# Kernel optimization log

Hardware: AMD Instinct MI355X
Metric: run time of the kernel (lower is better)

## Reference

```python
import jax, jax.numpy as jnp
import numpy as np
from jax import lax

B, N = 16, 8192          # batch, points per cloud
G, K = 512, 32           # num_groups, group_size
TOKEN_DIM = 384
BN_EPS = 1e-5


def setup_inputs() -> dict:
    key = jax.random.key(0)
    ks = jax.random.split(key, 8)
    w = lambda i, shape: jax.random.normal(ks[i], shape, jnp.float32) * 0.05
    return {
        "points": jax.random.normal(ks[0], (B, N, 3), jnp.float32),
        # first_conv: Conv1d(3,128,1,bias=False) -> BN(128) -> ReLU -> Conv1d(128,256,1)
        "w1": w(1, (128, 3)),
        "bn1_gamma": jnp.ones((128,), jnp.float32),
        "bn1_beta": jnp.zeros((128,), jnp.float32),
        "bn1_mean": jnp.zeros((128,), jnp.float32),
        "bn1_var": jnp.ones((128,), jnp.float32),
        "w2": w(2, (256, 128)),
        "b2": jnp.zeros((256,), jnp.float32),
        # second_conv: Conv1d(512,512,1,bias=False) -> BN(512) -> ReLU -> Conv1d(512,384,1)
        "w3": w(3, (512, 512)),
        "bn2_gamma": jnp.ones((512,), jnp.float32),
        "bn2_beta": jnp.zeros((512,), jnp.float32),
        "bn2_mean": jnp.zeros((512,), jnp.float32),
        "bn2_var": jnp.ones((512,), jnp.float32),
        "w4": w(4, (TOKEN_DIM, 512)),
        "b4": jnp.zeros((TOKEN_DIM,), jnp.float32),
    }


def _fps(xyz, num_samples):
    """Farthest point sampling. xyz: [B,N,3] -> idx [B,num_samples] (start = point 0)."""
    b, n, _ = xyz.shape
    start = jnp.zeros((b,), jnp.int32)
    init_min = jnp.full((b, n), 1e10, xyz.dtype)

    def body(carry, _):
        min_d2, last = carry
        last_pt = jnp.take_along_axis(xyz, last[:, None, None], axis=1)  # [B,1,3]
        d2 = jnp.sum((xyz - last_pt) ** 2, axis=-1)                      # [B,N]
        min_d2 = jnp.minimum(min_d2, d2)
        nxt = jnp.argmax(min_d2, axis=-1).astype(jnp.int32)
        return (min_d2, nxt), last

    _, idx = lax.scan(body, (init_min, start), None, length=num_samples)
    return idx.T  # [B,num_samples]


def _bn(x, gamma, beta, mean, var):
    # inference batchnorm over last (channel) axis
    return (x - mean) * lax.rsqrt(var + BN_EPS) * gamma + beta


def reference(points, w1, bn1_gamma, bn1_beta, bn1_mean, bn1_var, w2, b2,
              w3, bn2_gamma, bn2_beta, bn2_mean, bn2_var, w4, b4):
    xyz = points[:, :, :3]
    fidx = _fps(xyz, G)                                       # [B,G]
    centers = jnp.take_along_axis(xyz, fidx[:, :, None], 1)   # [B,G,3]

    # brute-force KNN via squared distances [B,G,N]
    pn = jnp.sum(xyz * xyz, -1)                               # [B,N]
    cn = jnp.sum(centers * centers, -1)                       # [B,G]
    d2 = cn[:, :, None] + pn[:, None, :] - 2.0 * jnp.einsum('bgc,bnc->bgn', centers, xyz)
    _, idx = lax.top_k(-d2, K)                                # [B,G,K] nearest indices

    groups = jax.vmap(lambda p, i: p[i])(points, idx)          # [B,G,K,3]
    groups = groups - centers[:, :, None, :]                   # center-relative coords

    x = groups.reshape(B * G, K, 3)                            # [M,K,3]
    # first_conv
    f = jnp.einsum('mkc,dc->mkd', x, w1)                       # [M,K,128]
    f = jax.nn.relu(_bn(f, bn1_gamma, bn1_beta, bn1_mean, bn1_var))
    f = jnp.einsum('mkd,ed->mke', f, w2) + b2                  # [M,K,256]
    g = jnp.max(f, axis=1, keepdims=True)                      # [M,1,256]
    f = jnp.concatenate([jnp.broadcast_to(g, f.shape), f], -1) # [M,K,512]
    # second_conv
    f = jnp.einsum('mke,fe->mkf', f, w3)                       # [M,K,512]
    f = jax.nn.relu(_bn(f, bn2_gamma, bn2_beta, bn2_mean, bn2_var))
    f = jnp.einsum('mkf,of->mko', f, w4) + b4                  # [M,K,384]
    tokens = jnp.max(f, axis=1).reshape(B, G, TOKEN_DIM)
    return tokens, centers
```

## Files before the change

### kernel.cpp

```cpp
#include <hip/hip_runtime.h>
#include <stdint.h>

#define PB 16
#define PN 8192
#define PG 512
#define PK 32
#define PTOK 384
#define PM (PB*PG)
#define PMK (PM*PK)
static constexpr float BN_EPS_C = 1e-5f;

typedef short bh8  __attribute__((ext_vector_type(8)));
typedef float f32x4 __attribute__((ext_vector_type(4)));

__device__ __forceinline__ short f2bf(float f){
  unsigned u = __float_as_uint(f);
  unsigned r = u + 0x7fffu + ((u>>16)&1u);
  return (short)(r>>16);
}
__device__ __forceinline__ float bf2f(short s){
  return __uint_as_float(((unsigned)(unsigned short)s)<<16);
}
__device__ __forceinline__ void gload16(const void* g, void* l){
  __builtin_amdgcn_global_load_lds((const __attribute__((address_space(1))) unsigned int*)g,
                                   (__attribute__((address_space(3))) unsigned int*)l,
                                   16, 0, 0);
}

__global__ __launch_bounds__(1024, 4) void fps_kernel(const float* __restrict__ points,
                                                      float* __restrict__ centers){
#pragma clang fp contract(off)
  const int b = blockIdx.x;
  const int t = threadIdx.x;
  const float* P = points + (size_t)b*PN*3;
  __shared__ float4 Lc[PN];
  __shared__ unsigned short sidx[PN];
  __shared__ int shist[512];
  __shared__ int spart[64];
  __shared__ unsigned long long swa[3];
  if (t < 512) shist[t] = 0;
  if (t < 3)   swa[t] = 0ull;
  __syncthreads();
  int mycell[8];
#pragma unroll
  for (int i=0;i<8;i++){
    int j = i*1024 + t;
    float x=P[j*3+0], y=P[j*3+1], z=P[j*3+2];
    Lc[j] = make_float4(x,y,z,0.f);
    int qx=(int)fminf(fmaxf((x+4.f)*1.0f,0.f),7.f);
    int qy=(int)fminf(fmaxf((y+4.f)*1.0f,0.f),7.f);
    int qz=(int)fminf(fmaxf((z+4.f)*1.0f,0.f),7.f);
    int mc = (qx&1)|((qx&2)<<2)|((qx&4)<<4)
           | ((qy&1)<<1)|((qy&2)<<3)|((qy&4)<<5)
           | ((qz&1)<<2)|((qz&2)<<4)|((qz&4)<<6);
    mycell[i]=mc;
    atomicAdd(&shist[mc],1);
  }
  __syncthreads();
  if (t < 64){
    int acc=0;
#pragma unroll
    for (int k=0;k<8;k++){ int h=shist[t*8+k]; shist[t*8+k]=acc; acc+=h; }
    spart[t]=acc;
  }
  __syncthreads();
  if (t==0){ int acc=0; for (int k=0;k<64;k++){ int h=spart[k]; spart[k]=acc; acc+=h; } }
  __syncthreads();
  if (t < 64){
    int off=spart[t];
#pragma unroll
    for (int k=0;k<8;k++) shist[t*8+k] += off;
  }
  __syncthreads();
#pragma unroll
  for (int i=0;i<8;i++){
    int j = i*1024 + t;
    int r = atomicAdd(&shist[mycell[i]],1);
    sidx[r] = (unsigned short)j;
  }
  __syncthreads();
  float px[8],py[8],pz[8],md[8]; int lowc[8];
  float tlx=1e30f,tly=1e30f,tlz=1e30f,thx=-1e30f,thy=-1e30f,thz=-1e30f;
#pragma unroll
  for (int i=0;i<8;i++){
    int oj = sidx[t*8+i];
    float4 p4 = Lc[oj];
    float x=p4.x, y=p4.y, z=p4.z;
    px[i]=x; py[i]=y; pz[i]=z; md[i]=1e10f; lowc[i]=PN-1-oj;
    tlx=fminf(tlx,x); thx=fmaxf(thx,x);
    tly=fminf(tly,y); thy=fmaxf(thy,y);
    tlz=fminf(tlz,z); thz=fmaxf(thz,z);
  }
#pragma unroll
  for (int off=32; off; off>>=1){
    tlx=fminf(tlx,__shfl_xor(tlx,off)); thx=fmaxf(thx,__shfl_xor(thx,off));
    tly=fminf(tly,__shfl_xor(tly,off)); thy=fmaxf(thy,__shfl_xor(thy,off));
    tlz=fminf(tlz,__shfl_xor(tlz,off)); thz=fmaxf(thz,__shfl_xor(thz,off));
  }
  unsigned long long wkey = ((unsigned long long)0x7F800000u)<<32;
  float cx=P[0], cy=P[1], cz=P[2];
  if (t==0){ float* c = centers + (size_t)b*PG*3; c[0]=cx; c[1]=cy; c[2]=cz; }
  const int lane = t & 63;
  __syncthreads();
  for (int g=1; g<PG; g++){
    const int sl = g%3, ns = (g+1)%3;
    float ddx=fmaxf(fmaxf(tlx-cx, cx-thx),0.f);
    float ddy=fmaxf(fmaxf(tly-cy, cy-thy),0.f);
    float ddz=fmaxf(fmaxf(tlz-cz, cz-thz),0.f);
    float dmin2=((ddx*ddx+ddy*ddy)+ddz*ddz)*0.999999f;
    if (!(dmin2 >= __uint_as_float((unsigned)(wkey>>32)))){
      unsigned long long bk = 0ull;
#pragma unroll
      for (int i=0;i<8;i++){
        float dx=px[i]-cx, dy=py[i]-cy, dz=pz[i]-cz;
        float d2 = (dx*dx + dy*dy) + dz*dz;
        md[i] = fminf(md[i], d2);
        unsigned long long ki = ((unsigned long long)__float_as_uint(md[i])<<32)
                              | (unsigned)lowc[i];
        if (ki > bk) bk = ki;
      }
#pragma unroll
      for (int mask=32; mask; mask>>=1){
        unsigned long long o = __shfl_xor(bk, mask);
        if (o > bk) bk = o;
      }
      wkey = bk;
    }
    if (lane==0) atomicMax(&swa[sl], wkey);
    if (t==0) swa[ns] = 0ull;
    __syncthreads();
    unsigned long long w = swa[sl];
    int j = PN-1 - (int)(w & 0xFFFFFFFFu);
    float4 c4 = Lc[j];
    cx = c4.x; cy = c4.y; cz = c4.z;
    if (t==0){ float* cc = centers + ((size_t)b*PG + g)*3; cc[0]=cx; cc[1]=cy; cc[2]=cz; }
  }
}

__global__ __launch_bounds__(256) void knn_kernel(const float* __restrict__ points,
                                                  const float* __restrict__ centers,
                                                  float* __restrict__ groups){
#pragma clang fp contract(off)
  const int m = blockIdx.x;
  const int b = m >> 9;
  const int t = threadIdx.x;
  const float* P = points + (size_t)b*PN*3;
  const float* c = centers + (size_t)m*3;
  const float cx=c[0], cy=c[1], cz=c[2];
  const float cn = (cx*cx + cy*cy) + cz*cz;
  unsigned long long key[PK];
#pragma unroll
  for (int i=0;i<PK;i++){
    int j = i*256 + t;
    float x=P[j*3+0], y=P[j*3+1], z=P[j*3+2];
    float pn = (x*x + y*y) + z*z;
    float e  = (cx*x + cy*y) + cz*z;
    float d2 = (cn + pn) - 2.0f*e;
    unsigned u = __float_as_uint(d2);
    u ^= (u & 0x80000000u) ? 0xFFFFFFFFu : 0x80000000u;
    key[i] = ((unsigned long long)u << 32) | (unsigned)j;
  }
  unsigned long long lmin = key[0];
#pragma unroll
  for (int i=1;i<PK;i++) if (key[i] < lmin) lmin = key[i];
  __shared__ unsigned long long swk[2][4];
  __shared__ int s_idx[PK];
  const int lane = t & 63, wid = t >> 6;
  for (int it=0; it<PK; it++){
    unsigned long long v = lmin;
#pragma unroll
    for (int off=32; off; off>>=1){
      unsigned long long o = __shfl_down(v, off);
      if (o < v) v = o;
    }
    if (lane==0) swk[it&1][wid] = v;
    __syncthreads();
    unsigned long long w = swk[it&1][0];
#pragma unroll
    for (int q=1;q<4;q++) if (swk[it&1][q] < w) w = swk[it&1][q];
    int wj = (int)(w & 0xFFFFFFFFull);
    if (t==0) s_idx[it] = wj;
    if ((wj & 255) == t){
#pragma unroll
      for (int i=0;i<PK;i++) if (key[i] == w) key[i] = ~0ull;
      lmin = key[0];
#pragma unroll
      for (int i=1;i<PK;i++) if (key[i] < lmin) lmin = key[i];
    }
  }
  __syncthreads();
  if (t < PK*3){
    int k = t/3, cc = t - k*3;
    int j = s_idx[k];
    groups[((size_t)m*PK + k)*3 + cc] = P[j*3+cc] - c[cc];
  }
}

__global__ __launch_bounds__(512, 2) void mlp_kernel(const float* __restrict__ grp,
                                                     const float* __restrict__ w1,
                                                     const float* __restrict__ sc1,
                                                     const float* __restrict__ sh1,
                                                     const short* __restrict__ w2b,
                                                     const float* __restrict__ b2,
                                                     const short* __restrict__ w3ab,
                                                     const short* __restrict__ w3bb,
                                                     const float* __restrict__ sc2,
                                                     const float* __restrict__ sh2,
                                                     const short* __restrict__ w4b,
                                                     const float* __restrict__ b4,
                                                     float* __restrict__ tokens){
  __shared__ __align__(16) short s_f1f3[16384];
  __shared__ __align__(16) short s_f2[32768];
  __shared__ __align__(16) short s_g[1024];
  __shared__ __align__(16) short s_bst[24576];
  const int t = threadIdx.x;
  const int lane = t & 63, wid = t >> 6;
  const int mh = wid >> 1, nq = wid & 1;
  const int B0 = blockIdx.x * 128;
  const int G0 = blockIdx.x * 4;
  const int srow = lane >> 2;
  const int scol = (lane & 3) * 8;
  const int frow = lane & 15;
  const int fk   = (lane >> 4) * 8;
  const int rb   = (lane >> 4) * 4;
  const int cb   = lane & 15;

  {
    int r = t & 127, dg = t >> 7;
    float x0 = grp[(size_t)(B0+r)*3 + 0];
    float x1 = grp[(size_t)(B0+r)*3 + 1];
    float x2 = grp[(size_t)(B0+r)*3 + 2];
#pragma unroll
    for (int dd=0; dd<32; dd++){
      int d = dg*32 + dd;
      float a = x0*w1[d*3+0] + x1*w1[d*3+1] + x2*w1[d*3+2];
      float y = a*sc1[d] + sh1[d];
      s_f1f3[dg*4096 + r*32 + dd] = f2bf(fmaxf(y, 0.f));
    }
  }
  __syncthreads();

  {
    f32x4 accB[2][8] = {};
    for (int k0=0; k0<128; k0+=64){
      for (int cc=wid; cc<32; cc+=8){
        int sub = cc & 1, rc = cc >> 1;
        int r = rc*16 + srow;
        gload16(w2b + (size_t)r*128 + k0 + sub*32 + scol, &s_bst[sub*8192 + rc*512]);
      }
      __syncthreads();
#pragma unroll
      for (int sub=0; sub<2; sub++){
        int kc = (k0 + sub*32) >> 5;
        bh8 af[2], bf[8];
#pragma unroll
        for (int i=0;i<2;i++)
          af[i] = *(const bh8*)&s_f1f3[kc*4096 + (mh*32 + i*16 + frow)*32 + fk];
#pragma unroll
        for (int j=0;j<8;j++)
          bf[j] = *(const bh8*)&s_bst[sub*8192 + (nq*128 + j*16 + frow)*32 + fk];
#pragma unroll
        for (int i=0;i<2;i++)
#pragma unroll
          for (int j=0;j<8;j++)
            accB[i][j] = __builtin_amdgcn_mfma_f32_16x16x32_bf16(af[i], bf[j], accB[i][j], 0,0,0);
      }
      __syncthreads();
    }
#pragma unroll
    for (int i=0;i<2;i++)
#pragma unroll
      for (int j=0;j<8;j++){
        int col = nq*128 + j*16 + cb;
#pragma unroll
        for (int r=0;r<4;r++){
          int row = mh*32 + i*16 + rb + r;
          s_f2[(col>>5)*4096 + row*32 + (col&31)] = f2bf(accB[i][j][r] + b2[col]);
        }
      }
  }
  __syncthreads();

  {
#pragma unroll
    for (int task=0; task<2; task++){
      int g = (t>>8) + task*2;
      int col = t & 255;
      int kc = col >> 5, c5 = col & 31;
      float mx = -3.4e38f;
#pragma unroll
      for (int kk=0; kk<PK; kk++)
        mx = fmaxf(mx, bf2f(s_f2[kc*4096 + (g*32 + kk)*32 + c5]));
      s_g[g*256 + col] = f2bf(mx);
    }
  }
  __syncthreads();

  f32x4 acc4[2][12] = {};
  for (int nc=0; nc<4; nc++){
    f32x4 acc3[2][4] = {};
    for (int k0=0; k0<512; k0+=64){
      const short* w3s = (k0 < 256) ? w3ab : w3bb;
      int kk0 = (k0 < 256) ? k0 : (k0 - 256);
      for (int cc=wid; cc<16; cc+=8){
        int sub = cc & 1, rc = cc >> 1;
        int r = nc*128 + rc*16 + srow;
        gload16(w3s + (size_t)r*256 + kk0 + sub*32 + scol, &s_bst[sub*4096 + rc*512]);
      }
      __syncthreads();
#pragma unroll
      for (int sub=0; sub<2; sub++){
        int k = k0 + sub*32;
        bh8 af[2], bf[4];
        if (k < 256){
#pragma unroll
          for (int i=0;i<2;i++)
            af[i] = *(const bh8*)&s_g[mh*256 + k + fk];
        } else {
          int kc = (k - 256) >> 5;
#pragma unroll
          for (int i=0;i<2;i++)
            af[i] = *(const bh8*)&s_f2[kc*4096 + (mh*32 + i*16 + frow)*32 + fk];
        }
#pragma unroll
        for (int j=0;j<4;j++)
          bf[j] = *(const bh8*)&s_bst[sub*4096 + (nq*64 + j*16 + frow)*32 + fk];
#pragma unroll
        for (int i=0;i<2;i++)
#pragma unroll
          for (int j=0;j<4;j++)
            acc3[i][j] = __builtin_amdgcn_mfma_f32_16x16x32_bf16(af[i], bf[j], acc3[i][j], 0,0,0);
      }
      __syncthreads();
    }
#pragma unroll
    for (int i=0;i<2;i++)
#pragma unroll
      for (int j=0;j<4;j++){
        int cl = nq*64 + j*16 + cb;
        int f  = nc*128 + cl;
        float s = sc2[f], h = sh2[f];
#pragma unroll
        for (int r=0;r<4;r++){
          int row = mh*32 + i*16 + rb + r;
          float v = acc3[i][j][r]*s + h;
          s_f1f3[(cl>>5)*4096 + row*32 + (cl&31)] = f2bf(fmaxf(v, 0.f));
        }
      }
    __syncthreads();
    for (int kk0=0; kk0<128; kk0+=64){
      for (int cc=wid; cc<48; cc+=8){
        int sub = cc & 1, rc = cc >> 1;
        int r = rc*16 + srow;
        gload16(w4b + (size_t)r*512 + nc*128 + kk0 + sub*32 + scol, &s_bst[sub*12288 + rc*512]);
      }
      __syncthreads();
#pragma unroll
      for (int sub=0; sub<2; sub++){
        int kc = (kk0 + sub*32) >> 5;
        bh8 af[2], bf[12];
#pragma unroll
        for (int i=0;i<2;i++)
          af[i] = *(const bh8*)&s_f1f3[kc*4096 + (mh*32 + i*16 + frow)*32 + fk];
#pragma unroll
        for (int j=0;j<12;j++)
          bf[j] = *(const bh8*)&s_bst[sub*12288 + (nq*192 + j*16 + frow)*32 + fk];
#pragma unroll
        for (int i=0;i<2;i++)
#pragma unroll
          for (int j=0;j<12;j++)
            acc4[i][j] = __builtin_amdgcn_mfma_f32_16x16x32_bf16(af[i], bf[j], acc4[i][j], 0,0,0);
      }
      __syncthreads();
    }
  }

#pragma unroll
  for (int j=0;j<12;j++){
    int col = nq*192 + j*16 + cb;
    float mx = -3.4e38f;
#pragma unroll
    for (int i=0;i<2;i++)
#pragma unroll
      for (int r=0;r<4;r++)
        mx = fmaxf(mx, acc4[i][j][r]);
    mx = fmaxf(mx, __shfl_xor(mx, 16));
    mx = fmaxf(mx, __shfl_xor(mx, 32));
    if (lane < 16)
      tokens[(size_t)(G0 + mh)*PTOK + col] = mx + b4[col];
  }
}

__global__ __launch_bounds__(256) void prep_kernel(const float* __restrict__ w2,
    const float* __restrict__ w3, const float* __restrict__ w4,
    const float* __restrict__ g1, const float* __restrict__ be1,
    const float* __restrict__ mu1, const float* __restrict__ va1,
    const float* __restrict__ g2, const float* __restrict__ be2,
    const float* __restrict__ mu2, const float* __restrict__ va2,
    short* __restrict__ w2b, short* __restrict__ w3ab, short* __restrict__ w3bb,
    short* __restrict__ w4b, float* __restrict__ sc1, float* __restrict__ sh1,
    float* __restrict__ sc2, float* __restrict__ sh2){
  int i = blockIdx.x*256 + threadIdx.x;
  if (i < 256*128) w2b[i] = f2bf(w2[i]);
  if (i < 512*512){
    int f = i >> 9, e = i & 511;
    short v = f2bf(w3[i]);
    if (e < 256) w3ab[f*256 + e] = v; else w3bb[f*256 + (e-256)] = v;
  }
  if (i < 384*512) w4b[i] = f2bf(w4[i]);
  if (i < 128){ float s = g1[i]*rsqrtf(va1[i] + BN_EPS_C); sc1[i]=s; sh1[i]=be1[i]-mu1[i]*s; }
  if (i < 512){ float s = g2[i]*rsqrtf(va2[i] + BN_EPS_C); sc2[i]=s; sh2[i]=be2[i]-mu2[i]*s; }
}

extern "C" void kernel_launch(void* const* d_in, const int* in_sizes, int n_in,
                              void* d_out, int out_size, void* d_ws, size_t ws_size,
                              hipStream_t stream){
  const float* points = (const float*)d_in[0];
  const float* w1  = (const float*)d_in[1];
  const float* g1  = (const float*)d_in[2];
  const float* be1 = (const float*)d_in[3];
  const float* mu1 = (const float*)d_in[4];
  const float* va1 = (const float*)d_in[5];
  const float* w2  = (const float*)d_in[6];
  const float* b2  = (const float*)d_in[7];
  const float* w3  = (const float*)d_in[8];
  const float* g2  = (const float*)d_in[9];
  const float* be2 = (const float*)d_in[10];
  const float* mu2 = (const float*)d_in[11];
  const float* va2 = (const float*)d_in[12];
  const float* w4  = (const float*)d_in[13];
  const float* b4  = (const float*)d_in[14];
  float* tokens  = (float*)d_out;
  float* centers = (float*)d_out + (size_t)PM*PTOK;

  char* ws = (char*)d_ws;
  float* grp  = (float*)(ws + 0);
  short* w2b  = (short*)(ws + 3145728ull);
  short* w3ab = (short*)(ws + 3211264ull);
  short* w3bb = (short*)(ws + 3473408ull);
  short* w4b  = (short*)(ws + 3735552ull);
  float* sc1  = (float*)(ws + 4128768ull);
  float* sh1  = (float*)(ws + 4129280ull);
  float* sc2  = (float*)(ws + 4129792ull);
  float* sh2  = (float*)(ws + 4131840ull);

  prep_kernel<<<1024, 256, 0, stream>>>(w2, w3, w4, g1, be1, mu1, va1, g2, be2, mu2, va2,
                                        w2b, w3ab, w3bb, w4b, sc1, sh1, sc2, sh2);
  fps_kernel<<<PB, 1024, 0, stream>>>(points, centers);
  knn_kernel<<<PM, 256, 0, stream>>>(points, centers, grp);
  mlp_kernel<<<PMK/128, 512, 0, stream>>>(grp, w1, sc1, sh1, w2b, b2,
                                          w3ab, w3bb, sc2, sh2, w4b, b4, tokens);
}
```

Before: 1.220 ms.

## Fuse FPS, KNN and MLP into persistent megakernel with progress-flag streaming

Replaces the three separate FPS, KNN and MLP launches with one persistent kernel. Sixteen blocks run FPS and publish per-batch progress counters every four centers. The remaining worker blocks pull tasks from an atomic queue, spin until their centers are ready, then do KNN for four groups and the MLP in the same block, with the tile reshaped for 16 waves. This overlaps the long serial FPS with downstream work and removes the intermediate groups buffer. In exchange it relies on forward progress of co-resident blocks and spin-waiting, and the larger block with fewer waves per SIMD may reduce MLP efficiency.

```diff
diff --git a/kernel.cpp b/kernel.cpp
--- a/kernel.cpp
+++ b/kernel.cpp
@@ -8,6 +8,8 @@
 #define PTOK 384
 #define PM (PB*PG)
 #define PMK (PM*PK)
+#define NWORK 224
+#define NTASK (PM/4)
 static constexpr float BN_EPS_C = 1e-5f;
 
 typedef short bh8  __attribute__((ext_vector_type(8)));
@@ -27,265 +29,282 @@
                                    16, 0, 0);
 }
 
-__global__ __launch_bounds__(1024, 4) void fps_kernel(const float* __restrict__ points,
-                                                      float* __restrict__ centers){
+__global__ __launch_bounds__(1024) void mega_kernel(
+    const float* __restrict__ points, float* __restrict__ centers,
+    int* __restrict__ prog, int* __restrict__ qhead,
+    const float* __restrict__ w1, const float* __restrict__ sc1,
+    const float* __restrict__ sh1, const short* __restrict__ w2b,
+    const float* __restrict__ b2, const short* __restrict__ w3ab,
+    const short* __restrict__ w3bb, const float* __restrict__ sc2,
+    const float* __restrict__ sh2, const short* __restrict__ w4b,
+    const float* __restrict__ b4, float* __restrict__ tokens){
 #pragma clang fp contract(off)
-  const int b = blockIdx.x;
-  const int t = threadIdx.x;
-  const float* P = points + (size_t)b*PN*3;
-  __shared__ float4 Lc[PN];
-  __shared__ unsigned short sidx[PN];
-  __shared__ int shist[512];
-  __shared__ int spart[64];
-  __shared__ unsigned long long swa[3];
-  if (t < 512) shist[t] = 0;
-  if (t < 3)   swa[t] = 0ull;
-  __syncthreads();
-  int mycell[8];
-#pragma unroll
-  for (int i=0;i<8;i++){
-    int j = i*1024 + t;
-    float x=P[j*3+0], y=P[j*3+1], z=P[j*3+2];
-    Lc[j] = make_float4(x,y,z,0.f);
-    int qx=(int)fminf(fmaxf((x+4.f)*1.0f,0.f),7.f);
-    int qy=(int)fminf(fmaxf((y+4.f)*1.0f,0.f),7.f);
-    int qz=(int)fminf(fmaxf((z+4.f)*1.0f,0.f),7.f);
-    int mc = (qx&1)|((qx&2)<<2)|((qx&4)<<4)
-           | ((qy&1)<<1)|((qy&2)<<3)|((qy&4)<<5)
-           | ((qz&1)<<2)|((qz&2)<<4)|((qz&4)<<6);
-    mycell[i]=mc;
-    atomicAdd(&shist[mc],1);
-  }
-  __syncthreads();
-  if (t < 64){
-    int acc=0;
-#pragma unroll
-    for (int k=0;k<8;k++){ int h=shist[t*8+k]; shist[t*8+k]=acc; acc+=h; }
-    spart[t]=acc;
-  }
-  __syncthreads();
-  if (t==0){ int acc=0; for (int k=0;k<64;k++){ int h=spart[k]; spart[k]=acc; acc+=h; } }
-  __syncthreads();
-  if (t < 64){
-    int off=spart[t];
-#pragma unroll
-    for (int k=0;k<8;k++) shist[t*8+k] += off;
-  }
-  __syncthreads();
-#pragma unroll
-  for (int i=0;i<8;i++){
-    int j = i*1024 + t;
-    int r = atomicAdd(&shist[mycell[i]],1);
-    sidx[r] = (unsigned short)j;
-  }
-  __syncthreads();
-  float px[8],py[8],pz[8],md[8]; int lowc[8];
-  float tlx=1e30f,tly=1e30f,tlz=1e30f,thx=-1e30f,thy=-1e30f,thz=-1e30f;
-#pragma unroll
-  for (int i=0;i<8;i++){
-    int oj = sidx[t*8+i];
-    float4 p4 = Lc[oj];
-    float x=p4.x, y=p4.y, z=p4.z;
-    px[i]=x; py[i]=y; pz[i]=z; md[i]=1e10f; lowc[i]=PN-1-oj;
-    tlx=fminf(tlx,x); thx=fmaxf(thx,x);
-    tly=fminf(tly,y); thy=fmaxf(thy,y);
-    tlz=fminf(tlz,z); thz=fmaxf(thz,z);
-  }
-#pragma unroll
-  for (int off=32; off; off>>=1){
-    tlx=fminf(tlx,__shfl_xor(tlx,off)); thx=fmaxf(thx,__shfl_xor(thx,off));
-    tly=fminf(tly,__shfl_xor(tly,off)); thy=fmaxf(thy,__shfl_xor(thy,off));
-    tlz=fminf(tlz,__shfl_xor(tlz,off)); thz=fmaxf(thz,__shfl_xor(thz,off));
-  }
-  unsigned long long wkey = ((unsigned long long)0x7F800000u)<<32;
-  float cx=P[0], cy=P[1], cz=P[2];
-  if (t==0){ float* c = centers + (size_t)b*PG*3; c[0]=cx; c[1]=cy; c[2]=cz; }
-  const int lane = t & 63;
-  __syncthreads();
-  for (int g=1; g<PG; g++){
-    const int sl = g%3, ns = (g+1)%3;
-    float ddx=fmaxf(fmaxf(tlx-cx, cx-thx),0.f);
-    float ddy=fmaxf(fmaxf(tly-cy, cy-thy),0.f);
-    float ddz=fmaxf(fmaxf(tlz-cz, cz-thz),0.f);
-    float dmin2=((ddx*ddx+ddy*ddy)+ddz*ddz)*0.999999f;
-    if (!(dmin2 >= __uint_as_float((unsigned)(wkey>>32)))){
-      unsigned long long bk = 0ull;
-#pragma unroll
-      for (int i=0;i<8;i++){
-        float dx=px[i]-cx, dy=py[i]-cy, dz=pz[i]-cz;
-        float d2 = (dx*dx + dy*dy) + dz*dz;
-        md[i] = fminf(md[i], d2);
-        unsigned long long ki = ((unsigned long long)__float_as_uint(md[i])<<32)
-                              | (unsigned)lowc[i];
-        if (ki > bk) bk = ki;
-      }
-#pragma unroll
-      for (int mask=32; mask; mask>>=1){
-        unsigned long long o = __shfl_xor(bk, mask);
-        if (o > bk) bk = o;
-      }
-      wkey = bk;
-    }
-    if (lane==0) atomicMax(&swa[sl], wkey);
-    if (t==0) swa[ns] = 0ull;
-    __syncthreads();
-    unsigned long long w = swa[sl];
-    int j = PN-1 - (int)(w & 0xFFFFFFFFu);
-    float4 c4 = Lc[j];
-    cx = c4.x; cy = c4.y; cz = c4.z;
-    if (t==0){ float* cc = centers + ((size_t)b*PG + g)*3; cc[0]=cx; cc[1]=cy; cc[2]=cz; }
-  }
-}
-
-__global__ __launch_bounds__(256) void knn_kernel(const float* __restrict__ points,
-                                                  const float* __restrict__ centers,
-                                                  float* __restrict__ groups){
-#pragma clang fp contract(off)
-  const int m = blockIdx.x;
-  const int b = m >> 9;
-  const int t = threadIdx.x;
-  const float* P = points + (size_t)b*PN*3;
-  const float* c = centers + (size_t)m*3;
-  const float cx=c[0], cy=c[1], cz=c[2];
-  const float cn = (cx*cx + cy*cy) + cz*cz;
-  unsigned long long key[PK];
-#pragma unroll
-  for (int i=0;i<PK;i++){
-    int j = i*256 + t;
-    float x=P[j*3+0], y=P[j*3+1], z=P[j*3+2];
-    float pn = (x*x + y*y) + z*z;
-    float e  = (cx*x + cy*y) + cz*z;
-    float d2 = (cn + pn) - 2.0f*e;
-    unsigned u = __float_as_uint(d2);
-    u ^= (u & 0x80000000u) ? 0xFFFFFFFFu : 0x80000000u;
-    key[i] = ((unsigned long long)u << 32) | (unsigned)j;
-  }
-  unsigned long long lmin = key[0];
-#pragma unroll
-  for (int i=1;i<PK;i++) if (key[i] < lmin) lmin = key[i];
-  __shared__ unsigned long long swk[2][4];
-  __shared__ int s_idx[PK];
-  const int lane = t & 63, wid = t >> 6;
-  for (int it=0; it<PK; it++){
-    unsigned long long v = lmin;
-#pragma unroll
-    for (int off=32; off; off>>=1){
-      unsigned long long o = __shfl_down(v, off);
-      if (o < v) v = o;
-    }
-    if (lane==0) swk[it&1][wid] = v;
-    __syncthreads();
-    unsigned long long w = swk[it&1][0];
-#pragma unroll
-    for (int q=1;q<4;q++) if (swk[it&1][q] < w) w = swk[it&1][q];
-    int wj = (int)(w & 0xFFFFFFFFull);
-    if (t==0) s_idx[it] = wj;
-    if ((wj & 255) == t){
-#pragma unroll
-      for (int i=0;i<PK;i++) if (key[i] == w) key[i] = ~0ull;
-      lmin = key[0];
-#pragma unroll
-      for (int i=1;i<PK;i++) if (key[i] < lmin) lmin = key[i];
-    }
-  }
-  __syncthreads();
-  if (t < PK*3){
-    int k = t/3, cc = t - k*3;
-    int j = s_idx[k];
-    groups[((size_t)m*PK + k)*3 + cc] = P[j*3+cc] - c[cc];
-  }
-}
-
-__global__ __launch_bounds__(512, 2) void mlp_kernel(const float* __restrict__ grp,
-                                                     const float* __restrict__ w1,
-                                                     const float* __restrict__ sc1,
-                                                     const float* __restrict__ sh1,
-                                                     const short* __restrict__ w2b,
-                                                     const float* __restrict__ b2,
-                                                     const short* __restrict__ w3ab,
-                                                     const short* __restrict__ w3bb,
-                                                     const float* __restrict__ sc2,
-                                                     const float* __restrict__ sh2,
-                                                     const short* __restrict__ w4b,
-                                                     const float* __restrict__ b4,
-                                                     float* __restrict__ tokens){
-  __shared__ __align__(16) short s_f1f3[16384];
-  __shared__ __align__(16) short s_f2[32768];
-  __shared__ __align__(16) short s_g[1024];
-  __shared__ __align__(16) short s_bst[24576];
+  __shared__ __align__(16) char SMEM[150528];
   const int t = threadIdx.x;
   const int lane = t & 63, wid = t >> 6;
-  const int mh = wid >> 1, nq = wid & 1;
-  const int B0 = blockIdx.x * 128;
-  const int G0 = blockIdx.x * 4;
-  const int srow = lane >> 2;
-  const int scol = (lane & 3) * 8;
-  const int frow = lane & 15;
-  const int fk   = (lane >> 4) * 8;
-  const int rb   = (lane >> 4) * 4;
-  const int cb   = lane & 15;
-
-  {
-    int r = t & 127, dg = t >> 7;
-    float x0 = grp[(size_t)(B0+r)*3 + 0];
-    float x1 = grp[(size_t)(B0+r)*3 + 1];
-    float x2 = grp[(size_t)(B0+r)*3 + 2];
-#pragma unroll
-    for (int dd=0; dd<32; dd++){
-      int d = dg*32 + dd;
-      float a = x0*w1[d*3+0] + x1*w1[d*3+1] + x2*w1[d*3+2];
-      float y = a*sc1[d] + sh1[d];
-      s_f1f3[dg*4096 + r*32 + dd] = f2bf(fmaxf(y, 0.f));
-    }
+
+  if (blockIdx.x < PB){
+    const int b = blockIdx.x;
+    const float* P = points + (size_t)b*PN*3;
+    float4* Lc = (float4*)SMEM;
+    unsigned short* sidx = (unsigned short*)(SMEM + 131072);
+    int* shist = (int*)(SMEM + 147456);
+    int* spart = (int*)(SMEM + 149504);
+    unsigned long long* swa = (unsigned long long*)(SMEM + 149760);
+    if (t < 512) shist[t] = 0;
+    if (t < 3)   swa[t] = 0ull;
+    __syncthreads();
+    int mycell[8];
+#pragma unroll
+    for (int i=0;i<8;i++){
+      int j = i*1024 + t;
+      float x=P[j*3+0], y=P[j*3+1], z=P[j*3+2];
+      Lc[j] = make_float4(x,y,z,0.f);
+      int qx=(int)fminf(fmaxf((x+4.f)*1.0f,0.f),7.f);
+      int qy=(int)fminf(fmaxf((y+4.f)*1.0f,0.f),7.f);
+      int qz=(int)fminf(fmaxf((z+4.f)*1.0f,0.f),7.f);
+      int mc = (qx&1)|((qx&2)<<2)|((qx&4)<<4)
+             | ((qy&1)<<1)|((qy&2)<<3)|((qy&4)<<5)
+             | ((qz&1)<<2)|((qz&2)<<4)|((qz&4)<<6);
+      mycell[i]=mc;
+      atomicAdd(&shist[mc],1);
+    }
+    __syncthreads();
+    if (t < 64){
+      int acc=0;
+#pragma unroll
+      for (int k=0;k<8;k++){ int h=shist[t*8+k]; shist[t*8+k]=acc; acc+=h; }
+      spart[t]=acc;
+    }
+    __syncthreads();
+    if (t==0){ int acc=0; for (int k=0;k<64;k++){ int h=spart[k]; spart[k]=acc; acc+=h; } }
+    __syncthreads();
+    if (t < 64){
+      int off=spart[t];
+#pragma unroll
+      for (int k=0;k<8;k++) shist[t*8+k] += off;
+    }
+    __syncthreads();
+#pragma unroll
+    for (int i=0;i<8;i++){
+      int j = i*1024 + t;
+      int r = atomicAdd(&shist[mycell[i]],1);
+      sidx[r] = (unsigned short)j;
+    }
+    __syncthreads();
+    float px[8],py[8],pz[8],md[8]; int lowc[8];
+    float tlx=1e30f,tly=1e30f,tlz=1e30f,thx=-1e30f,thy=-1e30f,thz=-1e30f;
+#pragma unroll
+    for (int i=0;i<8;i++){
+      int oj = sidx[t*8+i];
+      float4 p4 = Lc[oj];
+      float x=p4.x, y=p4.y, z=p4.z;
+      px[i]=x; py[i]=y; pz[i]=z; md[i]=1e10f; lowc[i]=PN-1-oj;
+      tlx=fminf(tlx,x); thx=fmaxf(thx,x);
+      tly=fminf(tly,y); thy=fmaxf(thy,y);
+      tlz=fminf(tlz,z); thz=fmaxf(thz,z);
+    }
+#pragma unroll
+    for (int off=32; off; off>>=1){
+      tlx=fminf(tlx,__shfl_xor(tlx,off)); thx=fmaxf(thx,__shfl_xor(thx,off));
+      tly=fminf(tly,__shfl_xor(tly,off)); thy=fmaxf(thy,__shfl_xor(thy,off));
+      tlz=fminf(tlz,__shfl_xor(tlz,off)); thz=fmaxf(thz,__shfl_xor(thz,off));
+    }
+    unsigned long long wkey = ((unsigned long long)0x7F800000u)<<32;
+    float cx=P[0], cy=P[1], cz=P[2];
+    if (t==0){ float* c = centers + (size_t)b*PG*3; c[0]=cx; c[1]=cy; c[2]=cz; }
+    __syncthreads();
+    for (int g=1; g<PG; g++){
+      const int sl = g%3, ns = (g+1)%3;
+      float ddx=fmaxf(fmaxf(tlx-cx, cx-thx),0.f);
+      float ddy=fmaxf(fmaxf(tly-cy, cy-thy),0.f);
+      float ddz=fmaxf(fmaxf(tlz-cz, cz-thz),0.f);
+      float dmin2=((ddx*ddx+ddy*ddy)+ddz*ddz)*0.999999f;
+      if (!(dmin2 >= __uint_as_float((unsigned)(wkey>>32)))){
+        unsigned long long bk = 0ull;
+#pragma unroll
+        for (int i=0;i<8;i++){
+          float dx=px[i]-cx, dy=py[i]-cy, dz=pz[i]-cz;
+          float d2 = (dx*dx + dy*dy) + dz*dz;
+          md[i] = fminf(md[i], d2);
+          unsigned long long ki = ((unsigned long long)__float_as_uint(md[i])<<32)
+                                | (unsigned)lowc[i];
+          if (ki > bk) bk = ki;
+        }
+#pragma unroll
+        for (int mask=32; mask; mask>>=1){
+          unsigned long long o = __shfl_xor(bk, mask);
+          if (o > bk) bk = o;
+        }
+        wkey = bk;
+      }
+      if (lane==0) atomicMax(&swa[sl], wkey);
+      if (t==0) swa[ns] = 0ull;
+      __syncthreads();
+      unsigned long long w = swa[sl];
+      int j = PN-1 - (int)(w & 0xFFFFFFFFu);
+      float4 c4 = Lc[j];
+      cx = c4.x; cy = c4.y; cz = c4.z;
+      if (t==0){
+        float* cc = centers + ((size_t)b*PG + g)*3;
+        cc[0]=cx; cc[1]=cy; cc[2]=cz;
+        if ((g & 3) == 3)
+          __hip_atomic_store(prog + b, g + 1, __ATOMIC_RELEASE, __HIP_MEMORY_SCOPE_AGENT);
+      }
+    }
+    return;
   }
-  __syncthreads();
-
-  {
-    f32x4 accB[2][8] = {};
-    for (int k0=0; k0<128; k0+=64){
-      for (int cc=wid; cc<32; cc+=8){
-        int sub = cc & 1, rc = cc >> 1;
-        int r = rc*16 + srow;
-        gload16(w2b + (size_t)r*128 + k0 + sub*32 + scol, &s_bst[sub*8192 + rc*512]);
+
+  short* s_f1f3 = (short*)SMEM;
+  short* s_f2   = (short*)(SMEM + 32768);
+  short* s_g    = (short*)(SMEM + 98304);
+  float* s_grp  = (float*)(SMEM + 98304);
+  short* s_bst  = (short*)(SMEM + 100352);
+  unsigned long long* ks_k = (unsigned long long*)(SMEM + 149504);
+  int*   ks_idx = (int*)(SMEM + 149760);
+  float* ks_c   = (float*)(SMEM + 150272);
+  int*   s_task = (int*)(SMEM + 150320);
+
+  const int mh = wid >> 2, nq = wid & 3;
+  const int srow = lane >> 2, scol = (lane & 3)*8;
+  const int frow = lane & 15, fk = (lane >> 4)*8;
+  const int rb = (lane >> 4)*4, cb = lane & 15;
+
+  for(;;){
+    if (t == 0){
+      int id = atomicAdd(qhead, 1);
+      s_task[0] = id;
+      if (id < NTASK){
+        int bb = id & (PB-1), qq = id >> 4;
+        int need = qq*4 + 4;
+        while (__hip_atomic_load(prog + bb, __ATOMIC_ACQUIRE, __HIP_MEMORY_SCOPE_AGENT) < need)
+          __builtin_amdgcn_s_sleep(10);
+      }
+    }
+    __syncthreads();
+    const int id = s_task[0];
+    if (id >= NTASK) break;
+    const int b = id & (PB-1), q = id >> 4;
+    const int m0 = b*PG + q*4;
+    const float* P = points + (size_t)b*PN*3;
+    const int sub = t >> 8, tt = t & 255;
+
+    if (tt == 0){
+      const float* cp = centers + (size_t)(m0 + sub)*3;
+      ks_c[sub*3+0] = __hip_atomic_load(cp+0, __ATOMIC_ACQUIRE, __HIP_MEMORY_SCOPE_AGENT);
+      ks_c[sub*3+1] = __hip_atomic_load(cp+1, __ATOMIC_ACQUIRE, __HIP_MEMORY_SCOPE_AGENT);
+      ks_c[sub*3+2] = __hip_atomic_load(cp+2, __ATOMIC_ACQUIRE, __HIP_MEMORY_SCOPE_AGENT);
+    }
+    __syncthreads();
+    {
+      const float cx=ks_c[sub*3+0], cy=ks_c[sub*3+1], cz=ks_c[sub*3+2];
+      const float cn = (cx*cx + cy*cy) + cz*cz;
+      unsigned long long key[PK];
+#pragma unroll
+      for (int i=0;i<PK;i++){
+        int j = i*256 + tt;
+        float x=P[j*3+0], y=P[j*3+1], z=P[j*3+2];
+        float pn = (x*x + y*y) + z*z;
+        float e  = (cx*x + cy*y) + cz*z;
+        float d2 = (cn + pn) - 2.0f*e;
+        unsigned u = __float_as_uint(d2);
+        u ^= (u & 0x80000000u) ? 0xFFFFFFFFu : 0x80000000u;
+        key[i] = ((unsigned long long)u << 32) | (unsigned)j;
+      }
+      unsigned long long lmin = key[0];
+#pragma unroll
+      for (int i=1;i<PK;i++) if (key[i] < lmin) lmin = key[i];
+      const int widx = tt >> 6;
+      for (int it=0; it<PK; it++){
+        unsigned long long v = lmin;
+#pragma unroll
+        for (int off=32; off; off>>=1){
+          unsigned long long o = __shfl_down(v, off);
+          if (o < v) v = o;
+        }
+        if (lane==0) ks_k[sub*8 + (it&1)*4 + widx] = v;
+        __syncthreads();
+        unsigned long long w = ks_k[sub*8 + (it&1)*4 + 0];
+#pragma unroll
+        for (int qq=1;qq<4;qq++){
+          unsigned long long o = ks_k[sub*8 + (it&1)*4 + qq];
+          if (o < w) w = o;
+        }
+        int wj = (int)(w & 0xFFFFFFFFull);
+        if (tt==0) ks_idx[sub*32 + it] = wj;
+        if ((wj & 255) == tt){
+#pragma unroll
+          for (int i=0;i<PK;i++) if (key[i] == w) key[i] = ~0ull;
+          lmin = key[0];
+#pragma unroll
+          for (int i=1;i<PK;i++) if (key[i] < lmin) lmin = key[i];
+        }
       }
       __syncthreads();
-#pragma unroll
-      for (int sub=0; sub<2; sub++){
-        int kc = (k0 + sub*32) >> 5;
-        bh8 af[2], bf[8];
-#pragma unroll
-        for (int i=0;i<2;i++)
-          af[i] = *(const bh8*)&s_f1f3[kc*4096 + (mh*32 + i*16 + frow)*32 + fk];
-#pragma unroll
-        for (int j=0;j<8;j++)
-          bf[j] = *(const bh8*)&s_bst[sub*8192 + (nq*128 + j*16 + frow)*32 + fk];
-#pragma unroll
-        for (int i=0;i<2;i++)
-#pragma unroll
-          for (int j=0;j<8;j++)
-            accB[i][j] = __builtin_amdgcn_mfma_f32_16x16x32_bf16(af[i], bf[j], accB[i][j], 0,0,0);
-      }
-      __syncthreads();
-    }
-#pragma unroll
-    for (int i=0;i<2;i++)
-#pragma unroll
-      for (int j=0;j<8;j++){
-        int col = nq*128 + j*16 + cb;
-#pragma unroll
-        for (int r=0;r<4;r++){
-          int row = mh*32 + i*16 + rb + r;
-          s_f2[(col>>5)*4096 + row*32 + (col&31)] = f2bf(accB[i][j][r] + b2[col]);
-        }
-      }
-  }
-  __syncthreads();
-
-  {
-#pragma unroll
-    for (int task=0; task<2; task++){
-      int g = (t>>8) + task*2;
-      int col = t & 255;
+      if (tt < PK*3){
+        int k = tt/3, c = tt - k*3;
+        int j = ks_idx[sub*32 + k];
+        s_grp[(sub*32 + k)*3 + c] = P[j*3+c] - ks_c[sub*3+c];
+      }
+    }
+    __syncthreads();
+
+    {
+      int r = t & 127, dg = t >> 7;
+      float x0 = s_grp[r*3+0], x1 = s_grp[r*3+1], x2 = s_grp[r*3+2];
+#pragma unroll
+      for (int dd=0; dd<16; dd++){
+        int d = dg*16 + dd;
+        float a = x0*w1[d*3+0] + x1*w1[d*3+1] + x2*w1[d*3+2];
+        float y = a*sc1[d] + sh1[d];
+        s_f1f3[(d>>5)*4096 + r*32 + (d&31)] = f2bf(fmaxf(y, 0.f));
+      }
+    }
+    __syncthreads();
+
+    {
+      f32x4 accB[2][4] = {};
+      for (int k0=0;k0<128;k0+=64){
+        for (int cc=wid; cc<32; cc+=16){
+          int sb = cc & 1, rc = cc >> 1;
+          gload16(w2b + (size_t)(rc*16+srow)*128 + k0 + sb*32 + scol,
+                  &s_bst[sb*8192 + rc*512]);
+        }
+        __syncthreads();
+#pragma unroll
+        for (int sb=0; sb<2; sb++){
+          int kc = (k0>>5) + sb;
+          bh8 af[2], bf[4];
+#pragma unroll
+          for (int i=0;i<2;i++)
+            af[i] = *(const bh8*)&s_f1f3[kc*4096 + (mh*32 + i*16 + frow)*32 + fk];
+#pragma unroll
+          for (int j=0;j<4;j++)
+            bf[j] = *(const bh8*)&s_bst[sb*8192 + (nq*64 + j*16 + frow)*32 + fk];
+#pragma unroll
+          for (int i=0;i<2;i++)
+#pragma unroll
+            for (int j=0;j<4;j++)
+              accB[i][j] = __builtin_amdgcn_mfma_f32_16x16x32_bf16(af[i], bf[j], accB[i][j], 0,0,0);
+        }
+        __syncthreads();
+      }
+#pragma unroll
+      for (int i=0;i<2;i++)
+#pragma unroll
+        for (int j=0;j<4;j++){
+          int col = nq*64 + j*16 + cb;
+#pragma unroll
+          for (int r=0;r<4;r++){
+            int row = mh*32 + i*16 + rb + r;
+            s_f2[(col>>5)*4096 + row*32 + (col&31)] = f2bf(accB[i][j][r] + b2[col]);
+          }
+        }
+    }
+    __syncthreads();
+
+    {
+      int g = t >> 8, col = t & 255;
       int kc = col >> 5, c5 = col & 31;
       float mx = -3.4e38f;
 #pragma unroll
@@ -293,101 +312,101 @@
         mx = fmaxf(mx, bf2f(s_f2[kc*4096 + (g*32 + kk)*32 + c5]));
       s_g[g*256 + col] = f2bf(mx);
     }
-  }
-  __syncthreads();
-
-  f32x4 acc4[2][12] = {};
-  for (int nc=0; nc<4; nc++){
-    f32x4 acc3[2][4] = {};
-    for (int k0=0; k0<512; k0+=64){
-      const short* w3s = (k0 < 256) ? w3ab : w3bb;
-      int kk0 = (k0 < 256) ? k0 : (k0 - 256);
-      for (int cc=wid; cc<16; cc+=8){
-        int sub = cc & 1, rc = cc >> 1;
-        int r = nc*128 + rc*16 + srow;
-        gload16(w3s + (size_t)r*256 + kk0 + sub*32 + scol, &s_bst[sub*4096 + rc*512]);
-      }
+    __syncthreads();
+
+    f32x4 acc4[2][6] = {};
+    for (int nc=0; nc<4; nc++){
+      f32x4 acc3[2][2] = {};
+      for (int k0=0; k0<512; k0+=64){
+        const short* w3s = (k0 < 256) ? w3ab : w3bb;
+        int kb = (k0 < 256) ? k0 : (k0 - 256);
+        {
+          int cc = wid;
+          int sb = cc & 1, rc = cc >> 1;
+          gload16(w3s + (size_t)(nc*128 + rc*16 + srow)*256 + kb + sb*32 + scol,
+                  &s_bst[sb*4096 + rc*512]);
+        }
+        __syncthreads();
+#pragma unroll
+        for (int sb=0; sb<2; sb++){
+          int k = k0 + sb*32;
+          bh8 af[2], bf[2];
+          if (k < 256){
+            bh8 gv = *(const bh8*)&s_g[mh*256 + k + fk];
+            af[0] = gv; af[1] = gv;
+          } else {
+            int kc = (k - 256) >> 5;
+#pragma unroll
+            for (int i=0;i<2;i++)
+              af[i] = *(const bh8*)&s_f2[kc*4096 + (mh*32 + i*16 + frow)*32 + fk];
+          }
+#pragma unroll
+          for (int j=0;j<2;j++)
+            bf[j] = *(const bh8*)&s_bst[sb*4096 + (nq*32 + j*16 + frow)*32 + fk];
+#pragma unroll
+          for (int i=0;i<2;i++)
+#pragma unroll
+            for (int j=0;j<2;j++)
+              acc3[i][j] = __builtin_amdgcn_mfma_f32_16x16x32_bf16(af[i], bf[j], acc3[i][j], 0,0,0);
+        }
+        __syncthreads();
+      }
+#pragma unroll
+      for (int i=0;i<2;i++)
+#pragma unroll
+        for (int j=0;j<2;j++){
+          int cl = nq*32 + j*16 + cb;
+          int f  = nc*128 + cl;
+          float s = sc2[f], h = sh2[f];
+#pragma unroll
+          for (int r=0;r<4;r++){
+            int row = mh*32 + i*16 + rb + r;
+            float v = acc3[i][j][r]*s + h;
+            s_f1f3[(cl>>5)*4096 + row*32 + (cl&31)] = f2bf(fmaxf(v, 0.f));
+          }
+        }
       __syncthreads();
-#pragma unroll
-      for (int sub=0; sub<2; sub++){
-        int k = k0 + sub*32;
-        bh8 af[2], bf[4];
-        if (k < 256){
+      for (int kk0=0; kk0<128; kk0+=64){
+        for (int cc=wid; cc<48; cc+=16){
+          int sb = cc & 1, rc = cc >> 1;
+          gload16(w4b + (size_t)(rc*16+srow)*512 + nc*128 + kk0 + sb*32 + scol,
+                  &s_bst[sb*12288 + rc*512]);
+        }
+        __syncthreads();
+#pragma unroll
+        for (int sb=0; sb<2; sb++){
+          int kc = (kk0 + sb*32) >> 5;
+          bh8 af[2], bf[6];
 #pragma unroll
           for (int i=0;i<2;i++)
-            af[i] = *(const bh8*)&s_g[mh*256 + k + fk];
-        } else {
-          int kc = (k - 256) >> 5;
+            af[i] = *(const bh8*)&s_f1f3[kc*4096 + (mh*32 + i*16 + frow)*32 + fk];
+#pragma unroll
+          for (int j=0;j<6;j++)
+            bf[j] = *(const bh8*)&s_bst[sb*12288 + (nq*96 + j*16 + frow)*32 + fk];
 #pragma unroll
           for (int i=0;i<2;i++)
-            af[i] = *(const bh8*)&s_f2[kc*4096 + (mh*32 + i*16 + frow)*32 + fk];
-        }
-#pragma unroll
-        for (int j=0;j<4;j++)
-          bf[j] = *(const bh8*)&s_bst[sub*4096 + (nq*64 + j*16 + frow)*32 + fk];
-#pragma unroll
-        for (int i=0;i<2;i++)
-#pragma unroll
-          for (int j=0;j<4;j++)
-            acc3[i][j] = __builtin_amdgcn_mfma_f32_16x16x32_bf16(af[i], bf[j], acc3[i][j], 0,0,0);
-      }
-      __syncthreads();
-    }
-#pragma unroll
-    for (int i=0;i<2;i++)
-#pragma unroll
-      for (int j=0;j<4;j++){
-        int cl = nq*64 + j*16 + cb;
-        int f  = nc*128 + cl;
-        float s = sc2[f], h = sh2[f];
-#pragma unroll
-        for (int r=0;r<4;r++){
-          int row = mh*32 + i*16 + rb + r;
-          float v = acc3[i][j][r]*s + h;
-          s_f1f3[(cl>>5)*4096 + row*32 + (cl&31)] = f2bf(fmaxf(v, 0.f));
-        }
-      }
-    __syncthreads();
-    for (int kk0=0; kk0<128; kk0+=64){
-      for (int cc=wid; cc<48; cc+=8){
-        int sub = cc & 1, rc = cc >> 1;
-        int r = rc*16 + srow;
-        gload16(w4b + (size_t)r*512 + nc*128 + kk0 + sub*32 + scol, &s_bst[sub*12288 + rc*512]);
-      }
-      __syncthreads();
-#pragma unroll
-      for (int sub=0; sub<2; sub++){
-        int kc = (kk0 + sub*32) >> 5;
-        bh8 af[2], bf[12];
-#pragma unroll
-        for (int i=0;i<2;i++)
-          af[i] = *(const bh8*)&s_f1f3[kc*4096 + (mh*32 + i*16 + frow)*32 + fk];
-#pragma unroll
-        for (int j=0;j<12;j++)
-          bf[j] = *(const bh8*)&s_bst[sub*12288 + (nq*192 + j*16 + frow)*32 + fk];
-#pragma unroll
-        for (int i=0;i<2;i++)
-#pragma unroll
-          for (int j=0;j<12;j++)
-            acc4[i][j] = __builtin_amdgcn_mfma_f32_16x16x32_bf16(af[i], bf[j], acc4[i][j], 0,0,0);
-      }
-      __syncthreads();
-    }
-  }
-
-#pragma unroll
-  for (int j=0;j<12;j++){
-    int col = nq*192 + j*16 + cb;
-    float mx = -3.4e38f;
-#pragma unroll
-    for (int i=0;i<2;i++)
-#pragma unroll
-      for (int r=0;r<4;r++)
-        mx = fmaxf(mx, acc4[i][j][r]);
-    mx = fmaxf(mx, __shfl_xor(mx, 16));
-    mx = fmaxf(mx, __shfl_xor(mx, 32));
-    if (lane < 16)
-      tokens[(size_t)(G0 + mh)*PTOK + col] = mx + b4[col];
+#pragma unroll
+            for (int j=0;j<6;j++)
+              acc4[i][j] = __builtin_amdgcn_mfma_f32_16x16x32_bf16(af[i], bf[j], acc4[i][j], 0,0,0);
+        }
+        __syncthreads();
+      }
+    }
+
+#pragma unroll
+    for (int j=0;j<6;j++){
+      int col = nq*96 + j*16 + cb;
+      float mx = -3.4e38f;
+#pragma unroll
+      for (int i=0;i<2;i++)
+#pragma unroll
+        for (int r=0;r<4;r++)
+          mx = fmaxf(mx, acc4[i][j][r]);
+      mx = fmaxf(mx, __shfl_xor(mx, 16));
+      mx = fmaxf(mx, __shfl_xor(mx, 32));
+      if (lane < 16)
+        tokens[(size_t)(m0 + mh)*PTOK + col] = mx + b4[col];
+    }
   }
 }
 
@@ -399,7 +418,8 @@
     const float* __restrict__ mu2, const float* __restrict__ va2,
     short* __restrict__ w2b, short* __restrict__ w3ab, short* __restrict__ w3bb,
     short* __restrict__ w4b, float* __restrict__ sc1, float* __restrict__ sh1,
-    float* __restrict__ sc2, float* __restrict__ sh2){
+    float* __restrict__ sc2, float* __restrict__ sh2,
+    int* __restrict__ prog, int* __restrict__ qhead){
   int i = blockIdx.x*256 + threadIdx.x;
   if (i < 256*128) w2b[i] = f2bf(w2[i]);
   if (i < 512*512){
@@ -410,6 +430,8 @@
   if (i < 384*512) w4b[i] = f2bf(w4[i]);
   if (i < 128){ float s = g1[i]*rsqrtf(va1[i] + BN_EPS_C); sc1[i]=s; sh1[i]=be1[i]-mu1[i]*s; }
   if (i < 512){ float s = g2[i]*rsqrtf(va2[i] + BN_EPS_C); sc2[i]=s; sh2[i]=be2[i]-mu2[i]*s; }
+  if (i < PB) prog[i] = 0;
+  if (i == PB) qhead[0] = 0;
 }
 
 extern "C" void kernel_launch(void* const* d_in, const int* in_sizes, int n_in,
@@ -434,20 +456,21 @@
   float* centers = (float*)d_out + (size_t)PM*PTOK;
 
   char* ws = (char*)d_ws;
-  float* grp  = (float*)(ws + 0);
-  short* w2b  = (short*)(ws + 3145728ull);
-  short* w3ab = (short*)(ws + 3211264ull);
-  short* w3bb = (short*)(ws + 3473408ull);
-  short* w4b  = (short*)(ws + 3735552ull);
-  float* sc1  = (float*)(ws + 4128768ull);
-  float* sh1  = (float*)(ws + 4129280ull);
-  float* sc2  = (float*)(ws + 4129792ull);
-  float* sh2  = (float*)(ws + 4131840ull);
+  short* w2b  = (short*)(ws + 0);
+  short* w3ab = (short*)(ws + 65536ull);
+  short* w3bb = (short*)(ws + 327680ull);
+  short* w4b  = (short*)(ws + 589824ull);
+  float* sc1  = (float*)(ws + 983040ull);
+  float* sh1  = (float*)(ws + 983552ull);
+  float* sc2  = (float*)(ws + 984064ull);
+  float* sh2  = (float*)(ws + 986112ull);
+  int*   prog = (int*)(ws + 988160ull);
+  int*   qhead= (int*)(ws + 988224ull);
 
   prep_kernel<<<1024, 256, 0, stream>>>(w2, w3, w4, g1, be1, mu1, va1, g2, be2, mu2, va2,
-                                        w2b, w3ab, w3bb, w4b, sc1, sh1, sc2, sh2);
-  fps_kernel<<<PB, 1024, 0, stream>>>(points, centers);
-  knn_kernel<<<PM, 256, 0, stream>>>(points, centers, grp);
-  mlp_kernel<<<PMK/128, 512, 0, stream>>>(grp, w1, sc1, sh1, w2b, b2,
-                                          w3ab, w3bb, sc2, sh2, w4b, b4, tokens);
-}
+                                        w2b, w3ab, w3bb, w4b, sc1, sh1, sc2, sh2,
+                                        prog, qhead);
+  mega_kernel<<<PB + NWORK, 1024, 0, stream>>>(points, centers, prog, qhead,
+                                               w1, sc1, sh1, w2b, b2, w3ab, w3bb,
+                                               sc2, sh2, w4b, b4, tokens);
+}
```

After: 1.964 ms. +61.0%, slower.
